# Kernel optimization log

Measured on AMD Instinct MI355X. Metric: run time of the kernel, lower is better.

Reference implementation:

```python
import jax, jax.numpy as jnp
import numpy as np

N = 20000   # nodes
E = 320000  # edges
NE = 2000   # entities
H = 4       # attention heads
D = 128     # hidden_dim (per-head out feats)
K = 10      # knn k


def _gat(h, src, dst, W, al, ar, Wr, relu):
    # h: [N, Fin]; W: [H*D, Fin]; al/ar: [H, D]; Wr: [H*D, Fin]
    feat = (h @ W.T).reshape(N, H, D)                      # [N,H,D]
    el = jnp.sum(feat * al[None], axis=-1)                 # [N,H]
    er = jnp.sum(feat * ar[None], axis=-1)                 # [N,H]
    e = jax.nn.leaky_relu(el[src] + er[dst], 0.2)          # [E,H]
    emax = jax.ops.segment_max(e, dst, num_segments=N)
    emax = jnp.where(jnp.isfinite(emax), emax, 0.0)
    a = jnp.exp(e - emax[dst])                             # [E,H]
    asum = jax.ops.segment_sum(a, dst, num_segments=N)
    asum = jnp.where(asum > 0, asum, 1.0)
    alpha = a / asum[dst]                                  # edge softmax over incoming edges
    msg = alpha[:, :, None] * feat[src]                    # [E,H,D]
    rst = jax.ops.segment_sum(msg, dst, num_segments=N)    # [N,H,D]
    rst = rst + (h @ Wr.T).reshape(N, H, D)                # residual
    if relu:
        rst = jax.nn.relu(rst)
    return rst


def _mlp2(x, W1, b1, W2, b2):
    return jax.nn.sigmoid(jax.nn.relu(x @ W1.T + b1) @ W2.T + b2)


def setup_inputs() -> dict:
    key = jax.random.key(0)
    ks = jax.random.split(key, 32)
    f32 = jnp.float32
    p = lambda i, s: (jax.random.normal(ks[i], s, dtype=f32) * 0.05)
    inp = {
        'position': jax.random.normal(ks[0], (N, 2), dtype=f32),
        'w_embed': jax.random.normal(ks[1], (N, 126), dtype=f32),
        'src': jax.random.randint(ks[2], (E,), 0, N),
        'dst': jax.random.randint(ks[3], (E,), 0, N),
        'entity': jax.random.randint(ks[4], (N,), 0, NE),
        # GAT layer 1 (in=128)
        'W1': p(5, (H * D, 128)), 'al1': p(6, (H, D)), 'ar1': p(7, (H, D)), 'Wr1': p(8, (H * D, 128)),
        # GAT layer 2 (in=512)
        'W2': p(9, (H * D, H * D)), 'al2': p(10, (H, D)), 'ar2': p(11, (H, D)), 'Wr2': p(12, (H * D, H * D)),
        # GAT layer 3 (in=512)
        'W3': p(13, (H * D, H * D)), 'al3': p(14, (H, D)), 'ar3': p(15, (H, D)), 'Wr3': p(16, (H * D, H * D)),
        # w_group_mlp
        'Wg1': p(17, (D, D)), 'bg1': p(18, (D,)), 'Wg2': p(19, (1, D)), 'bg2': p(20, (1,)),
        # entity_linear
        'We': p(21, (D, D)), 'be': p(22, (D,)),
        # entity_link_mlp
        'Wl1': p(23, (D, D)), 'bl1': p(24, (D,)), 'Wl2': p(25, (1, D)), 'bl2': p(26, (1,)),
        # entity_classify
        'Wc': p(27, (4, D)), 'bc': p(28, (4,)),
    }
    return inp


def reference(position, w_embed, src, dst, entity,
              W1, al1, ar1, Wr1, W2, al2, ar2, Wr2, W3, al3, ar3, Wr3,
              Wg1, bg1, Wg2, bg2, We, be, Wl1, bl1, Wl2, bl2, Wc, bc):
    h = jnp.concatenate([position, w_embed], axis=1)        # [N,128]
    h = _gat(h, src, dst, W1, al1, ar1, Wr1, True).reshape(N, H * D)
    h = _gat(h, src, dst, W2, al2, ar2, Wr2, True).reshape(N, H * D)
    h = _gat(h, src, dst, W3, al3, ar3, Wr3, False).mean(axis=1)  # [N,D]

    # pairwise group score over edges
    groups_score = _mlp2(jnp.abs(h[src] - h[dst]), Wg1, bg1, Wg2, bg2).squeeze(-1)  # [E]

    # per-entity segment reduce
    ent_sum = jax.ops.segment_sum(h, entity, num_segments=NE)            # [NE,D]
    entity_states = ent_sum @ We.T + be                                  # [NE,D]
    pos_sum = jax.ops.segment_sum(position, entity, num_segments=NE)     # [NE,2]
    cnt = jax.ops.segment_sum(jnp.ones((N,), jnp.float32), entity, num_segments=NE)
    entity_positions = pos_sum / jnp.maximum(cnt, 1.0)[:, None]          # [NE,2]

    # knn graph on entity centroids (k=10, includes self like dgl.knn_graph)
    d2 = jnp.sum((entity_positions[:, None, :] - entity_positions[None, :, :]) ** 2, axis=-1)  # [NE,NE]
    _, knn_idx = jax.lax.top_k(-d2, K)                                   # [NE,K]
    src_e = knn_idx.reshape(-1)                                          # [NE*K]
    dst_e = jnp.repeat(jnp.arange(NE), K)
    entity_link_score = _mlp2(jnp.abs(entity_states[src_e] - entity_states[dst_e]),
                              Wl1, bl1, Wl2, bl2).squeeze(-1)            # [NE*K]

    entity_class = jax.nn.sigmoid(entity_states @ Wc.T + bc)             # [NE,4]
    return (groups_score, entity_class, entity_positions, entity_link_score)
```

## Files before the change

kernel.cpp:

```cpp
#include <hip/hip_runtime.h>
#include <math.h>

#define N_NODES 20000
#define N_EDGES 320000
#define NENT    2000
#define KNN_K   10

typedef __attribute__((ext_vector_type(4))) float f32x4;
typedef __attribute__((ext_vector_type(8))) short bf16x8;
typedef __attribute__((ext_vector_type(8))) unsigned short u16x8;
typedef __attribute__((ext_vector_type(4))) unsigned short u16x4;

__device__ __forceinline__ unsigned short f2bf(float f) {
  union { float f; unsigned u; } v; v.f = f;
  unsigned r = v.u + 0x7fffu + ((v.u >> 16) & 1u);
  return (unsigned short)(r >> 16);
}
__device__ __forceinline__ float bf2f(unsigned short u) {
  union { unsigned u; float f; } v; v.u = ((unsigned)u) << 16;
  return v.f;
}
__device__ __forceinline__ float sigmoidf(float x) {
  return 1.f / (1.f + __expf(-x));
}
__device__ __forceinline__ void gload_lds16(const unsigned short* g, unsigned short* lds) {
  __builtin_amdgcn_global_load_lds(
      (const __attribute__((address_space(1))) unsigned int*)g,
      (__attribute__((address_space(3))) unsigned int*)lds, 16, 0, 0);
}

__global__ void k_build_h0(const float* __restrict__ pos, const float* __restrict__ wemb,
                           unsigned short* __restrict__ h0) {
  int i = blockIdx.x * blockDim.x + threadIdx.x;
  if (i >= N_NODES * 128) return;
  int n = i >> 7, c = i & 127;
  float v = (c < 2) ? pos[n * 2 + c] : wemb[n * 126 + (c - 2)];
  h0[i] = f2bf(v);
}

__global__ void k_f2bf(const float* __restrict__ in, unsigned short* __restrict__ out, int n) {
  int i = blockIdx.x * blockDim.x + threadIdx.x;
  if (i * 4 >= n) return;
  f32x4 v = *(const f32x4*)(in + i * 4);
  u16x4 o;
  o[0] = f2bf(v[0]); o[1] = f2bf(v[1]); o[2] = f2bf(v[2]); o[3] = f2bf(v[3]);
  *(u16x4*)(out + i * 4) = o;
}

__global__ __launch_bounds__(256) void k_gemm_bt(
    const unsigned short* __restrict__ A, const unsigned short* __restrict__ B,
    unsigned short* __restrict__ C, int M, int Nc, int K) {
  __shared__ __align__(16) unsigned short As[128 * 64];
  __shared__ __align__(16) unsigned short Bs[128 * 64];
  const int bm = blockIdx.x * 128, bn = blockIdx.y * 128;
  const int t = threadIdx.x;
  const int l = t & 63, w = t >> 6;
  const int wr = w >> 1, wc = w & 1;
  f32x4 acc[4][4];
#pragma unroll
  for (int m = 0; m < 4; ++m)
#pragma unroll
    for (int n = 0; n < 4; ++n) acc[m][n] = (f32x4){0.f, 0.f, 0.f, 0.f};

  for (int kb = 0; kb < K; kb += 64) {
    __syncthreads();
#pragma unroll
    for (int i = 0; i < 4; ++i) {
      int c = t + 256 * i;
      int row = c >> 3, cc = c & 7;
      int scc = cc ^ (row & 7);
      int ar = bm + row; if (ar > M - 1) ar = M - 1;
      gload_lds16(A + (size_t)ar * K + kb + scc * 8, &As[(size_t)(w * 64 + 256 * i) * 8]);
      gload_lds16(B + (size_t)(bn + row) * K + kb + scc * 8,
                  &Bs[(size_t)(w * 64 + 256 * i) * 8]);
    }
    __syncthreads();
#pragma unroll
    for (int kk = 0; kk < 2; ++kk) {
      bf16x8 af[4], bfr[4];
#pragma unroll
      for (int m = 0; m < 4; ++m) {
        int row = wr * 64 + m * 16 + (l & 15);
        int g = (kk * 4 + (l >> 4)) ^ (row & 7);
        af[m] = *(const bf16x8*)&As[row * 64 + g * 8];
      }
#pragma unroll
      for (int n = 0; n < 4; ++n) {
        int row = wc * 64 + n * 16 + (l & 15);
        int g = (kk * 4 + (l >> 4)) ^ (row & 7);
        bfr[n] = *(const bf16x8*)&Bs[row * 64 + g * 8];
      }
#pragma unroll
      for (int m = 0; m < 4; ++m)
#pragma unroll
        for (int n = 0; n < 4; ++n)
          acc[m][n] = __builtin_amdgcn_mfma_f32_16x16x32_bf16(af[m], bfr[n], acc[m][n], 0, 0, 0);
    }
  }
#pragma unroll
  for (int m = 0; m < 4; ++m) {
    int r0 = bm + wr * 64 + m * 16 + ((l >> 4) << 2);
#pragma unroll
    for (int n = 0; n < 4; ++n) {
      int c0 = bn + wc * 64 + n * 16 + (l & 15);
#pragma unroll
      for (int r = 0; r < 4; ++r) {
        int row = r0 + r;
        if (row < M) C[(size_t)row * Nc + c0] = f2bf(acc[m][n][r]);
      }
    }
  }
}

__global__ void k_el_er(const unsigned short* __restrict__ feat, int fstride,
                        const float* __restrict__ al, const float* __restrict__ ar,
                        float* __restrict__ el, float* __restrict__ er) {
  int wid = (blockIdx.x * blockDim.x + threadIdx.x) >> 6;
  if (wid >= N_NODES) return;
  int l = threadIdx.x & 63;
  int g = l >> 4, q = l & 15;
  u16x8 fv = *(const u16x8*)(feat + (size_t)wid * fstride + l * 8);
  const float* alp = al + g * 128 + q * 8;
  const float* arp = ar + g * 128 + q * 8;
  float sl = 0.f, sr = 0.f;
#pragma unroll
  for (int j = 0; j < 8; ++j) { float f = bf2f(fv[j]); sl += f * alp[j]; sr += f * arp[j]; }
#pragma unroll
  for (int d = 1; d < 16; d <<= 1) { sl += __shfl_xor(sl, d); sr += __shfl_xor(sr, d); }
  if (q == 0) { el[wid * 4 + g] = sl; er[wid * 4 + g] = sr; }
}

__global__ void k_hist(const int* __restrict__ dst, int* __restrict__ indeg) {
  int e = blockIdx.x * blockDim.x + threadIdx.x;
  if (e < N_EDGES) atomicAdd(&indeg[dst[e]], 1);
}

__global__ __launch_bounds__(1024) void k_scan_fast(const int* __restrict__ indeg,
                                                    int* __restrict__ indptr,
                                                    int* __restrict__ cursor) {
  __shared__ int wsum[16];
  const int t = threadIdx.x;
  const int l = t & 63, w = t >> 6;
  const int CH = 20;
  int base = t * CH;
  int vals[CH];
  int s = 0;
#pragma unroll
  for (int i = 0; i < CH; ++i) {
    int idx = base + i;
    int v = (idx < N_NODES) ? indeg[idx] : 0;
    vals[i] = v;
    s += v;
  }
  int ss = s;
#pragma unroll
  for (int d = 1; d < 64; d <<= 1) { int o = __shfl_up(ss, d); if (l >= d) ss += o; }
  if (l == 63) wsum[w] = ss;
  __syncthreads();
  if (t < 16) {
    int v = wsum[t];
#pragma unroll
    for (int d = 1; d < 16; d <<= 1) { int o = __shfl_up(v, d); if (t >= d) v += o; }
    wsum[t] = v;
  }
  __syncthreads();
  int run = ((w > 0) ? wsum[w - 1] : 0) + ss - s;
  if (t == 0) indptr[0] = 0;
#pragma unroll
  for (int i = 0; i < CH; ++i) {
    int idx = base + i;
    if (idx < N_NODES) {
      cursor[idx] = run;
      run += vals[i];
      indptr[idx + 1] = run;
    }
  }
}

__global__ void k_scatter(const int* __restrict__ src, const int* __restrict__ dst,
                          int* __restrict__ cursor, int* __restrict__ csr_src) {
  int e = blockIdx.x * blockDim.x + threadIdx.x;
  if (e < N_EDGES) {
    int p = atomicAdd(&cursor[dst[e]], 1);
    csr_src[p] = src[e];
  }
}

template <bool FINAL>
__global__ void k_gat_agg(const unsigned short* __restrict__ feat,
                          const unsigned short* __restrict__ hres, int fstride,
                          const float* __restrict__ el, const float* __restrict__ er,
                          const int* __restrict__ indptr, const int* __restrict__ csr_src,
                          unsigned short* __restrict__ hnext, float* __restrict__ h3,
                          unsigned short* __restrict__ h3b) {
  int wid = (blockIdx.x * blockDim.x + threadIdx.x) >> 6;
  if (wid >= N_NODES) return;
  int l = threadIdx.x & 63;
  int g = l >> 4;
  int beg = indptr[wid], end = indptr[wid + 1];
  f32x4 er4 = *(const f32x4*)(er + wid * 4);
  const float NI = -__builtin_inff();
  f32x4 mx = (f32x4){NI, NI, NI, NI};
  for (int j = beg + l; j < end; j += 64) {
    int s = csr_src[j];
    f32x4 el4 = *(const f32x4*)(el + s * 4);
#pragma unroll
    for (int h = 0; h < 4; ++h) {
      float v = el4[h] + er4[h];
      v = (v >= 0.f) ? v : 0.2f * v;
      mx[h] = fmaxf(mx[h], v);
    }
  }
#pragma unroll
  for (int d = 1; d < 64; d <<= 1) {
#pragma unroll
    for (int h = 0; h < 4; ++h) mx[h] = fmaxf(mx[h], __shfl_xor(mx[h], d));
  }
  float m_g = mx[g];
  float er_g = er4[g];
  float asum = 0.f;
  float acc[8];
#pragma unroll
  for (int j2 = 0; j2 < 8; ++j2) acc[j2] = 0.f;
  const unsigned short* fbase = feat + l * 8;
  int j = beg;
  for (; j + 4 <= end; j += 4) {
    int s0 = csr_src[j + 0], s1 = csr_src[j + 1];
    int s2 = csr_src[j + 2], s3 = csr_src[j + 3];
    float q0 = el[s0 * 4 + g], q1 = el[s1 * 4 + g];
    float q2 = el[s2 * 4 + g], q3 = el[s3 * 4 + g];
    u16x8 f0 = *(const u16x8*)(fbase + (size_t)s0 * fstride);
    u16x8 f1 = *(const u16x8*)(fbase + (size_t)s1 * fstride);
    u16x8 f2 = *(const u16x8*)(fbase + (size_t)s2 * fstride);
    u16x8 f3 = *(const u16x8*)(fbase + (size_t)s3 * fstride);
    float e0 = q0 + er_g; e0 = (e0 >= 0.f) ? e0 : 0.2f * e0;
    float e1 = q1 + er_g; e1 = (e1 >= 0.f) ? e1 : 0.2f * e1;
    float e2 = q2 + er_g; e2 = (e2 >= 0.f) ? e2 : 0.2f * e2;
    float e3 = q3 + er_g; e3 = (e3 >= 0.f) ? e3 : 0.2f * e3;
    float p0 = __expf(e0 - m_g), p1 = __expf(e1 - m_g);
    float p2 = __expf(e2 - m_g), p3 = __expf(e3 - m_g);
    asum += (p0 + p1) + (p2 + p3);
#pragma unroll
    for (int k = 0; k < 8; ++k)
      acc[k] += p0 * bf2f(f0[k]) + p1 * bf2f(f1[k]) + p2 * bf2f(f2[k]) + p3 * bf2f(f3[k]);
  }
  for (; j < end; ++j) {
    int s = csr_src[j];
    float ev = el[s * 4 + g] + er_g;
    ev = (ev >= 0.f) ? ev : 0.2f * ev;
    float p = __expf(ev - m_g);
    asum += p;
    u16x8 fv = *(const u16x8*)(fbase + (size_t)s * fstride);
#pragma unroll
    for (int k = 0; k < 8; ++k) acc[k] += p * bf2f(fv[k]);
  }
  float inv = (end > beg) ? 1.f / asum : 1.f;
  u16x8 hv = *(const u16x8*)(hres + (size_t)wid * fstride + l * 8);
  float o[8];
#pragma unroll
  for (int k = 0; k < 8; ++k) o[k] = acc[k] * inv + bf2f(hv[k]);
  if constexpr (!FINAL) {
    u16x8 ob;
#pragma unroll
    for (int k = 0; k < 8; ++k) ob[k] = f2bf(fmaxf(o[k], 0.f));
    *(u16x8*)(hnext + (size_t)wid * 512 + l * 8) = ob;
  } else {
#pragma unroll
    for (int k = 0; k < 8; ++k) {
      float v = o[k];
      v += __shfl_xor(v, 16);
      v += __shfl_xor(v, 32);
      o[k] = v * 0.25f;
    }
    if (g == 0) {
      f32x4 o0 = (f32x4){o[0], o[1], o[2], o[3]};
      f32x4 o1 = (f32x4){o[4], o[5], o[6], o[7]};
      *(f32x4*)(h3 + (size_t)wid * 128 + l * 8) = o0;
      *(f32x4*)(h3 + (size_t)wid * 128 + l * 8 + 4) = o1;
      u16x8 hb;
#pragma unroll
      for (int k = 0; k < 8; ++k) hb[k] = f2bf(o[k]);
      *(u16x8*)(h3b + (size_t)wid * 128 + l * 8) = hb;
    }
  }
}

template <int MODE>
__global__ __launch_bounds__(256) void k_pair_mlp(
    const unsigned short* __restrict__ X, const int* __restrict__ ia,
    const int* __restrict__ ib, const unsigned short* __restrict__ Wb,
    const float* __restrict__ b1, const float* __restrict__ W2,
    const float* __restrict__ b2, float* __restrict__ out, int npairs) {
  __shared__ __align__(16) unsigned short Xs[128 * 128];
  const int t = threadIdx.x;
  const int l = t & 63, w = t >> 6, wr = w >> 1, wc = w & 1;
  const int e0 = blockIdx.x * 128;
  {
    int r = t >> 1, hf = t & 1;
    int e = e0 + r;
    if (MODE == 1 && e >= npairs) e = npairs - 1;
    int sa, sb;
    if (MODE == 0) { sa = ia[e]; sb = ib[e]; }
    else           { sa = ia[e]; sb = e / KNN_K; }
    const unsigned short* pa = X + (size_t)sa * 128 + hf * 64;
    const unsigned short* pb = X + (size_t)sb * 128 + hf * 64;
#pragma unroll
    for (int c = 0; c < 64; c += 8) {
      u16x8 av = *(const u16x8*)(pa + c);
      u16x8 bv = *(const u16x8*)(pb + c);
      u16x8 xv;
#pragma unroll
      for (int j = 0; j < 8; ++j) xv[j] = f2bf(fabsf(bf2f(av[j]) - bf2f(bv[j])));
      int gb = hf * 8 + (c >> 3);
      *(u16x8*)&Xs[r * 128 + (gb ^ (r & 15)) * 8] = xv;
    }
  }
  __syncthreads();
  f32x4 acc[4][4];
#pragma unroll
  for (int m = 0; m < 4; ++m)
#pragma unroll
    for (int n = 0; n < 4; ++n) acc[m][n] = (f32x4){0.f, 0.f, 0.f, 0.f};
#pragma unroll
  for (int kk = 0; kk < 4; ++kk) {
    bf16x8 af[4], bfr[4];
#pragma unroll
    for (int n = 0; n < 4; ++n) {
      int rowv = wc * 64 + n * 16 + (l & 15);
      bfr[n] = *(const bf16x8*)(Wb + (size_t)rowv * 128 + (kk * 4 + (l >> 4)) * 8);
    }
#pragma unroll
    for (int m = 0; m < 4; ++m) {
      int row = wr * 64 + m * 16 + (l & 15);
      int gsw = (kk * 4 + (l >> 4)) ^ (row & 15);
      af[m] = *(const bf16x8*)&Xs[row * 128 + gsw * 8];
    }
#pragma unroll
    for (int m = 0; m < 4; ++m)
#pragma unroll
      for (int n = 0; n < 4; ++n)
        acc[m][n] = __builtin_amdgcn_mfma_f32_16x16x32_bf16(af[m], bfr[n], acc[m][n], 0, 0, 0);
  }
  float part[4][4];
#pragma unroll
  for (int m = 0; m < 4; ++m)
#pragma unroll
    for (int r = 0; r < 4; ++r) part[m][r] = 0.f;
#pragma unroll
  for (int n = 0; n < 4; ++n) {
    int col = wc * 64 + n * 16 + (l & 15);
    float bb = b1[col], w2 = W2[col];
#pragma unroll
    for (int m = 0; m < 4; ++m)
#pragma unroll
      for (int r = 0; r < 4; ++r) {
        float y = fmaxf(acc[m][n][r] + bb, 0.f);
        part[m][r] += y * w2;
      }
  }
#pragma unroll
  for (int d = 1; d < 16; d <<= 1)
#pragma unroll
    for (int m = 0; m < 4; ++m)
#pragma unroll
      for (int r = 0; r < 4; ++r) part[m][r] += __shfl_xor(part[m][r], d);
  __syncthreads();
  float* sc = (float*)Xs;
  if ((l & 15) == 0) {
#pragma unroll
    for (int m = 0; m < 4; ++m)
#pragma unroll
      for (int r = 0; r < 4; ++r)
        sc[wc * 128 + wr * 64 + m * 16 + (l >> 4) * 4 + r] = part[m][r];
  }
  __syncthreads();
  if (t < 128 && (MODE == 0 || e0 + t < npairs)) {
    float logit = sc[t] + sc[128 + t] + b2[0];
    out[e0 + t] = sigmoidf(logit);
  }
}

__global__ void k_ent_scatter(const float* __restrict__ h3, const float* __restrict__ pos,
                              const int* __restrict__ entity, float* __restrict__ ent_sum,
                              float* __restrict__ pos_sum, float* __restrict__ cnt) {
  int i = blockIdx.x * blockDim.x + threadIdx.x;
  if (i >= N_NODES * 32) return;
  int n = i >> 5, c = i & 31;
  int e = entity[n];
  f32x4 v = *(const f32x4*)(h3 + (size_t)n * 128 + c * 4);
  atomicAdd(&ent_sum[e * 128 + c * 4 + 0], v[0]);
  atomicAdd(&ent_sum[e * 128 + c * 4 + 1], v[1]);
  atomicAdd(&ent_sum[e * 128 + c * 4 + 2], v[2]);
  atomicAdd(&ent_sum[e * 128 + c * 4 + 3], v[3]);
  if (c == 0) {
    atomicAdd(&pos_sum[e * 2 + 0], pos[n * 2 + 0]);
    atomicAdd(&pos_sum[e * 2 + 1], pos[n * 2 + 1]);
    atomicAdd(&cnt[e], 1.f);
  }
}

__global__ void k_entity_states(const float* __restrict__ ent_sum, const float* __restrict__ We,
                                const float* __restrict__ be, float* __restrict__ es) {
  int i = blockIdx.x * blockDim.x + threadIdx.x;
  if (i >= NENT * 128) return;
  int e = i >> 7, j = i & 127;
  const float* x = ent_sum + (size_t)e * 128;
  const float* wrow = We + (size_t)j * 128;
  float s = be[j];
  for (int k = 0; k < 128; k += 4) {
    f32x4 xv = *(const f32x4*)(x + k);
    f32x4 wv = *(const f32x4*)(wrow + k);
    s += xv[0] * wv[0] + xv[1] * wv[1] + xv[2] * wv[2] + xv[3] * wv[3];
  }
  es[i] = s;
}

__global__ void k_entity_class(const float* __restrict__ es, const float* __restrict__ Wc,
                               const float* __restrict__ bc, float* __restrict__ out) {
  int i = blockIdx.x * blockDim.x + threadIdx.x;
  if (i >= NENT * 4) return;
  int e = i >> 2, c = i & 3;
  const float* x = es + (size_t)e * 128;
  const float* wrow = Wc + (size_t)c * 128;
  float s = bc[c];
  for (int k = 0; k < 128; ++k) s += x[k] * wrow[k];
  out[i] = sigmoidf(s);
}

__global__ void k_entity_pos(const float* __restrict__ pos_sum, const float* __restrict__ cnt,
                             float* __restrict__ outpos, float* __restrict__ wspos) {
  int e = blockIdx.x * blockDim.x + threadIdx.x;
  if (e >= NENT) return;
  float c = fmaxf(cnt[e], 1.f);
  float x = pos_sum[e * 2] / c, y = pos_sum[e * 2 + 1] / c;
  outpos[e * 2] = x; outpos[e * 2 + 1] = y;
  wspos[e * 2] = x; wspos[e * 2 + 1] = y;
}

__global__ __launch_bounds__(256) void k_knn(const float* __restrict__ entpos,
                                             int* __restrict__ knn) {
  __shared__ float d2row[NENT];
  __shared__ float rv[256];
  __shared__ int ri[256];
  int i = blockIdx.x, t = threadIdx.x;
  float px = entpos[i * 2], py = entpos[i * 2 + 1];
  for (int j = t; j < NENT; j += 256) {
    float dx = px - entpos[j * 2], dy = py - entpos[j * 2 + 1];
    d2row[j] = __fadd_rn(__fmul_rn(dx, dx), __fmul_rn(dy, dy));
  }
  __syncthreads();
  for (int k = 0; k < KNN_K; ++k) {
    float bv = __builtin_inff(); int bi = 0x7fffffff;
    for (int j = t; j < NENT; j += 256) {
      float v = d2row[j];
      if (v < bv) { bv = v; bi = j; }
    }
    rv[t] = bv; ri[t] = bi;
    __syncthreads();
    for (int s = 128; s > 0; s >>= 1) {
      if (t < s) {
        if (rv[t + s] < rv[t] || (rv[t + s] == rv[t] && ri[t + s] < ri[t])) {
          rv[t] = rv[t + s]; ri[t] = ri[t + s];
        }
      }
      __syncthreads();
    }
    if (t == 0) { knn[i * KNN_K + k] = ri[0]; d2row[ri[0]] = __builtin_inff(); }
    __syncthreads();
  }
}

extern "C" void kernel_launch(void* const* d_in, const int* in_sizes, int n_in,
                              void* d_out, int out_size, void* d_ws, size_t ws_size,
                              hipStream_t stream) {
  const float* position = (const float*)d_in[0];
  const float* w_embed  = (const float*)d_in[1];
  const int*   src      = (const int*)d_in[2];
  const int*   dst      = (const int*)d_in[3];
  const int*   entity   = (const int*)d_in[4];
  const float* W1 = (const float*)d_in[5];
  const float* al1 = (const float*)d_in[6];
  const float* ar1 = (const float*)d_in[7];
  const float* Wr1 = (const float*)d_in[8];
  const float* W2 = (const float*)d_in[9];
  const float* al2 = (const float*)d_in[10];
  const float* ar2 = (const float*)d_in[11];
  const float* Wr2 = (const float*)d_in[12];
  const float* W3 = (const float*)d_in[13];
  const float* al3 = (const float*)d_in[14];
  const float* ar3 = (const float*)d_in[15];
  const float* Wr3 = (const float*)d_in[16];
  const float* Wg1 = (const float*)d_in[17];
  const float* bg1 = (const float*)d_in[18];
  const float* Wg2 = (const float*)d_in[19];
  const float* bg2 = (const float*)d_in[20];
  const float* We  = (const float*)d_in[21];
  const float* be  = (const float*)d_in[22];
  const float* Wl1 = (const float*)d_in[23];
  const float* bl1 = (const float*)d_in[24];
  const float* Wl2 = (const float*)d_in[25];
  const float* bl2 = (const float*)d_in[26];
  const float* Wc  = (const float*)d_in[27];
  const float* bc  = (const float*)d_in[28];

  float* out_groups = (float*)d_out;
  float* out_class  = out_groups + N_EDGES;
  float* out_pos    = out_class + NENT * 4;
  float* out_link   = out_pos + NENT * 2;

  char* ws = (char*)d_ws;
  size_t off = 0;
  auto carve = [&](size_t bytes) -> char* {
    char* p = ws + off;
    off = (off + bytes + 255) & ~(size_t)255;
    return p;
  };
  unsigned short* featC = (unsigned short*)carve((size_t)N_NODES * 1024 * 2);
  unsigned short* hA = (unsigned short*)carve((size_t)N_NODES * 512 * 2);
  unsigned short* hB = (unsigned short*)carve((size_t)N_NODES * 512 * 2);
  unsigned short* wbf = (unsigned short*)carve((size_t)1024 * 512 * 2);
  unsigned short* wg1b = (unsigned short*)carve(128 * 128 * 2);
  unsigned short* wl1b = (unsigned short*)carve(128 * 128 * 2);
  float* el = (float*)carve((size_t)N_NODES * 4 * 4);
  float* er = (float*)carve((size_t)N_NODES * 4 * 4);
  int* indeg = (int*)carve((size_t)N_NODES * 4);
  int* indptr = (int*)carve((size_t)(N_NODES + 1) * 4);
  int* cursor = (int*)carve((size_t)N_NODES * 4);
  int* csr_src = (int*)carve((size_t)N_EDGES * 4);
  float* h3 = (float*)carve((size_t)N_NODES * 128 * 4);
  unsigned short* h3b = (unsigned short*)carve((size_t)N_NODES * 128 * 2);
  float* ent_sum = (float*)carve((size_t)NENT * 128 * 4);
  float* pos_sum = (float*)carve((size_t)NENT * 2 * 4);
  float* cnt = (float*)carve((size_t)NENT * 4);
  float* es = (float*)carve((size_t)NENT * 128 * 4);
  unsigned short* esb = (unsigned short*)carve((size_t)NENT * 128 * 2);
  float* wspos = (float*)carve((size_t)NENT * 2 * 4);
  int* knn = (int*)carve((size_t)NENT * KNN_K * 4);

  hipMemsetAsync(indeg, 0, (size_t)N_NODES * 4, stream);
  k_hist<<<(N_EDGES + 255) / 256, 256, 0, stream>>>(dst, indeg);
  k_scan_fast<<<1, 1024, 0, stream>>>(indeg, indptr, cursor);
  k_scatter<<<(N_EDGES + 255) / 256, 256, 0, stream>>>(src, dst, cursor, csr_src);

  k_build_h0<<<(N_NODES * 128 + 255) / 256, 256, 0, stream>>>(position, w_embed, hA);

  dim3 ggrid((N_NODES + 127) / 128, 8), gblk(256);

  k_f2bf<<<(512 * 128 / 4 + 255) / 256, 256, 0, stream>>>(W1, wbf, 512 * 128);
  k_f2bf<<<(512 * 128 / 4 + 255) / 256, 256, 0, stream>>>(Wr1, wbf + 512 * 128, 512 * 128);
  k_gemm_bt<<<ggrid, gblk, 0, stream>>>(hA, wbf, featC, N_NODES, 1024, 128);
  k_el_er<<<5000, 256, 0, stream>>>(featC, 1024, al1, ar1, el, er);
  k_gat_agg<false><<<5000, 256, 0, stream>>>(featC, featC + 512, 1024, el, er, indptr,
                                             csr_src, hB, nullptr, nullptr);

  k_f2bf<<<(512 * 512 / 4 + 255) / 256, 256, 0, stream>>>(W2, wbf, 512 * 512);
  k_f2bf<<<(512 * 512 / 4 + 255) / 256, 256, 0, stream>>>(Wr2, wbf + 512 * 512, 512 * 512);
  k_gemm_bt<<<ggrid, gblk, 0, stream>>>(hB, wbf, featC, N_NODES, 1024, 512);
  k_el_er<<<5000, 256, 0, stream>>>(featC, 1024, al2, ar2, el, er);
  k_gat_agg<false><<<5000, 256, 0, stream>>>(featC, featC + 512, 1024, el, er, indptr,
                                             csr_src, hA, nullptr, nullptr);

  k_f2bf<<<(512 * 512 / 4 + 255) / 256, 256, 0, stream>>>(W3, wbf, 512 * 512);
  k_f2bf<<<(512 * 512 / 4 + 255) / 256, 256, 0, stream>>>(Wr3, wbf + 512 * 512, 512 * 512);
  k_gemm_bt<<<ggrid, gblk, 0, stream>>>(hA, wbf, featC, N_NODES, 1024, 512);
  k_el_er<<<5000, 256, 0, stream>>>(featC, 1024, al3, ar3, el, er);
  k_gat_agg<true><<<5000, 256, 0, stream>>>(featC, featC + 512, 1024, el, er, indptr,
                                            csr_src, nullptr, h3, h3b);

  k_f2bf<<<(128 * 128 / 4 + 255) / 256, 256, 0, stream>>>(Wg1, wg1b, 128 * 128);
  k_pair_mlp<0><<<N_EDGES / 128, 256, 0, stream>>>(h3b, src, dst, wg1b, bg1, Wg2, bg2,
                                                   out_groups, N_EDGES);

  hipMemsetAsync(ent_sum, 0, (size_t)NENT * 128 * 4, stream);
  hipMemsetAsync(pos_sum, 0, (size_t)NENT * 2 * 4, stream);
  hipMemsetAsync(cnt, 0, (size_t)NENT * 4, stream);
  k_ent_scatter<<<(N_NODES * 32 + 255) / 256, 256, 0, stream>>>(h3, position, entity, ent_sum,
                                                                pos_sum, cnt);
  k_entity_states<<<(NENT * 128 + 255) / 256, 256, 0, stream>>>(ent_sum, We, be, es);
  k_entity_class<<<(NENT * 4 + 255) / 256, 256, 0, stream>>>(es, Wc, bc, out_class);
  k_entity_pos<<<(NENT + 255) / 256, 256, 0, stream>>>(pos_sum, cnt, out_pos, wspos);
  k_knn<<<NENT, 256, 0, stream>>>(wspos, knn);
  k_f2bf<<<(NENT * 128 / 4 + 255) / 256, 256, 0, stream>>>(es, esb, NENT * 128);
  k_f2bf<<<(128 * 128 / 4 + 255) / 256, 256, 0, stream>>>(Wl1, wl1b, 128 * 128);
  k_pair_mlp<1><<<(NENT * KNN_K + 127) / 128, 256, 0, stream>>>(esb, knn, nullptr, wl1b, bl1,
                                                                Wl2, bl2, out_link,
                                                                NENT * KNN_K);
}
```

Measured before the change: 497.4 us.

## Restructure pair MLP so each wave owns 32 pairs and streams W1 columns

The pair-MLP kernel now gives each wave its own 32-row slab of absolute-difference features in shared memory, keeps its A fragments in registers, and loops over all 128 hidden columns in 16-wide chunks. The next W1 chunk is prefetched from global while the current one is used, and the cross-wave shared-memory reduction plus its extra barriers are removed in favour of per-wave vectorised output stores. This cuts accumulator registers and inter-wave synchronisation and may raise occupancy. The cost is that every wave reads the whole weight matrix rather than half of it, and the launch grid for the entity-link call is resized to match.

```diff
diff --git a/kernel.cpp b/kernel.cpp
--- a/kernel.cpp
+++ b/kernel.cpp
@@ -291,92 +291,96 @@
     const int* __restrict__ ib, const unsigned short* __restrict__ Wb,
     const float* __restrict__ b1, const float* __restrict__ W2,
     const float* __restrict__ b2, float* __restrict__ out, int npairs) {
-  __shared__ __align__(16) unsigned short Xs[128 * 128];
+  __shared__ __align__(16) unsigned short Xs[4][32 * 128];
   const int t = threadIdx.x;
-  const int l = t & 63, w = t >> 6, wr = w >> 1, wc = w & 1;
-  const int e0 = blockIdx.x * 128;
+  const int l = t & 63, w = t >> 6;
+  unsigned short* xs = Xs[w];
+  const int base = (blockIdx.x * 4 + w) * 32;
   {
-    int r = t >> 1, hf = t & 1;
-    int e = e0 + r;
-    if (MODE == 1 && e >= npairs) e = npairs - 1;
+    int e = base + (l >> 1);
+    if (e >= npairs) e = npairs - 1;
     int sa, sb;
     if (MODE == 0) { sa = ia[e]; sb = ib[e]; }
     else           { sa = ia[e]; sb = e / KNN_K; }
+    int hf = l & 1, el = l >> 1;
     const unsigned short* pa = X + (size_t)sa * 128 + hf * 64;
     const unsigned short* pb = X + (size_t)sb * 128 + hf * 64;
 #pragma unroll
-    for (int c = 0; c < 64; c += 8) {
-      u16x8 av = *(const u16x8*)(pa + c);
-      u16x8 bv = *(const u16x8*)(pb + c);
+    for (int c = 0; c < 8; ++c) {
+      u16x8 av = *(const u16x8*)(pa + c * 8);
+      u16x8 bv = *(const u16x8*)(pb + c * 8);
       u16x8 xv;
 #pragma unroll
       for (int j = 0; j < 8; ++j) xv[j] = f2bf(fabsf(bf2f(av[j]) - bf2f(bv[j])));
-      int gb = hf * 8 + (c >> 3);
-      *(u16x8*)&Xs[r * 128 + (gb ^ (r & 15)) * 8] = xv;
+      int sg = (hf * 8 + c) ^ (el & 15);
+      *(u16x8*)&xs[el * 128 + sg * 8] = xv;
     }
   }
   __syncthreads();
-  f32x4 acc[4][4];
-#pragma unroll
-  for (int m = 0; m < 4; ++m)
-#pragma unroll
-    for (int n = 0; n < 4; ++n) acc[m][n] = (f32x4){0.f, 0.f, 0.f, 0.f};
-#pragma unroll
-  for (int kk = 0; kk < 4; ++kk) {
-    bf16x8 af[4], bfr[4];
-#pragma unroll
-    for (int n = 0; n < 4; ++n) {
-      int rowv = wc * 64 + n * 16 + (l & 15);
-      bfr[n] = *(const bf16x8*)(Wb + (size_t)rowv * 128 + (kk * 4 + (l >> 4)) * 8);
-    }
-#pragma unroll
-    for (int m = 0; m < 4; ++m) {
-      int row = wr * 64 + m * 16 + (l & 15);
-      int gsw = (kk * 4 + (l >> 4)) ^ (row & 15);
-      af[m] = *(const bf16x8*)&Xs[row * 128 + gsw * 8];
-    }
-#pragma unroll
-    for (int m = 0; m < 4; ++m)
-#pragma unroll
-      for (int n = 0; n < 4; ++n)
-        acc[m][n] = __builtin_amdgcn_mfma_f32_16x16x32_bf16(af[m], bfr[n], acc[m][n], 0, 0, 0);
-  }
-  float part[4][4];
-#pragma unroll
-  for (int m = 0; m < 4; ++m)
+  bf16x8 af[2][4];
+#pragma unroll
+  for (int m = 0; m < 2; ++m)
+#pragma unroll
+    for (int kk = 0; kk < 4; ++kk) {
+      int row = m * 16 + (l & 15);
+      int sg = (kk * 4 + (l >> 4)) ^ (row & 15);
+      af[m][kk] = *(const bf16x8*)&xs[row * 128 + sg * 8];
+    }
+  const size_t wlane = (size_t)(l & 15) * 128 + (l >> 4) * 8;
+  bf16x8 bcur[4], bnext[4];
+#pragma unroll
+  for (int kk = 0; kk < 4; ++kk)
+    bcur[kk] = *(const bf16x8*)(Wb + wlane + kk * 32);
+  float part[2][4];
+#pragma unroll
+  for (int m = 0; m < 2; ++m)
 #pragma unroll
     for (int r = 0; r < 4; ++r) part[m][r] = 0.f;
 #pragma unroll
-  for (int n = 0; n < 4; ++n) {
-    int col = wc * 64 + n * 16 + (l & 15);
-    float bb = b1[col], w2 = W2[col];
-#pragma unroll
-    for (int m = 0; m < 4; ++m)
-#pragma unroll
-      for (int r = 0; r < 4; ++r) {
-        float y = fmaxf(acc[m][n][r] + bb, 0.f);
-        part[m][r] += y * w2;
+  for (int n = 0; n < 8; ++n) {
+    if (n < 7) {
+#pragma unroll
+      for (int kk = 0; kk < 4; ++kk)
+        bnext[kk] = *(const bf16x8*)(Wb + wlane + (size_t)(n + 1) * 2048 + kk * 32);
+    }
+    f32x4 acc0 = (f32x4){0.f, 0.f, 0.f, 0.f};
+    f32x4 acc1 = (f32x4){0.f, 0.f, 0.f, 0.f};
+#pragma unroll
+    for (int kk = 0; kk < 4; ++kk) {
+      acc0 = __builtin_amdgcn_mfma_f32_16x16x32_bf16(af[0][kk], bcur[kk], acc0, 0, 0, 0);
+      acc1 = __builtin_amdgcn_mfma_f32_16x16x32_bf16(af[1][kk], bcur[kk], acc1, 0, 0, 0);
+    }
+    int col = n * 16 + (l & 15);
+    float bb = b1[col], w2v = W2[col];
+#pragma unroll
+    for (int r = 0; r < 4; ++r) {
+      part[0][r] += fmaxf(acc0[r] + bb, 0.f) * w2v;
+      part[1][r] += fmaxf(acc1[r] + bb, 0.f) * w2v;
+    }
+#pragma unroll
+    for (int kk = 0; kk < 4; ++kk) bcur[kk] = bnext[kk];
+  }
+#pragma unroll
+  for (int d = 1; d < 16; d <<= 1)
+#pragma unroll
+    for (int m = 0; m < 2; ++m)
+#pragma unroll
+      for (int r = 0; r < 4; ++r) part[m][r] += __shfl_xor(part[m][r], d);
+  if ((l & 15) == 0) {
+    int q = l >> 4;
+    float b2v = b2[0];
+#pragma unroll
+    for (int m = 0; m < 2; ++m) {
+      int e = base + m * 16 + q * 4;
+      f32x4 ov;
+#pragma unroll
+      for (int r = 0; r < 4; ++r) ov[r] = sigmoidf(part[m][r] + b2v);
+      if (e + 3 < npairs) *(f32x4*)(out + e) = ov;
+      else {
+#pragma unroll
+        for (int r = 0; r < 4; ++r) if (e + r < npairs) out[e + r] = ov[r];
       }
-  }
-#pragma unroll
-  for (int d = 1; d < 16; d <<= 1)
-#pragma unroll
-    for (int m = 0; m < 4; ++m)
-#pragma unroll
-      for (int r = 0; r < 4; ++r) part[m][r] += __shfl_xor(part[m][r], d);
-  __syncthreads();
-  float* sc = (float*)Xs;
-  if ((l & 15) == 0) {
-#pragma unroll
-    for (int m = 0; m < 4; ++m)
-#pragma unroll
-      for (int r = 0; r < 4; ++r)
-        sc[wc * 128 + wr * 64 + m * 16 + (l >> 4) * 4 + r] = part[m][r];
-  }
-  __syncthreads();
-  if (t < 128 && (MODE == 0 || e0 + t < npairs)) {
-    float logit = sc[t] + sc[128 + t] + b2[0];
-    out[e0 + t] = sigmoidf(logit);
+    }
   }
 }
 
@@ -582,7 +586,7 @@
   k_knn<<<NENT, 256, 0, stream>>>(wspos, knn);
   k_f2bf<<<(NENT * 128 / 4 + 255) / 256, 256, 0, stream>>>(es, esb, NENT * 128);
   k_f2bf<<<(128 * 128 / 4 + 255) / 256, 256, 0, stream>>>(Wl1, wl1b, 128 * 128);
-  k_pair_mlp<1><<<(NENT * KNN_K + 127) / 128, 256, 0, stream>>>(esb, knn, nullptr, wl1b, bl1,
-                                                                Wl2, bl2, out_link,
-                                                                NENT * KNN_K);
-}
+  k_pair_mlp<1><<<(NENT * KNN_K / 32 + 3) / 4, 256, 0, stream>>>(esb, knn, nullptr, wl1b, bl1,
+                                                                 Wl2, bl2, out_link,
+                                                                 NENT * KNN_K);
+}
```

New measurement: 511.7 us. 1.03x slower.
